# Optimization experiments

Hardware: AMD Instinct MI355X
Metric: run time of the kernel (lower is better)

Reference implementation:

```python
import jax, jax.numpy as jnp
import numpy as np

B, S, DM = 4, 2048, 1024
H, HD = 16, 64  # num_heads, head_dimension


def setup_inputs() -> dict:
    key = jax.random.key(0)
    ks = jax.random.split(key, 11)
    s = 0.02
    return {
        "queries": jax.random.normal(ks[0], (B, S, DM), dtype=jnp.float32),
        "keys": jax.random.normal(ks[1], (B, S, DM), dtype=jnp.float32),
        "values": jax.random.normal(ks[2], (B, S, DM), dtype=jnp.float32),
        # projection params, stored [in, out] (transpose of torch Linear weight)
        "Wq": jax.random.normal(ks[3], (DM, H * HD), dtype=jnp.float32) * s,
        "bq": jnp.zeros((H * HD,), dtype=jnp.float32),
        "Wk": jax.random.normal(ks[4], (DM, H * HD), dtype=jnp.float32) * s,
        "bk": jnp.zeros((H * HD,), dtype=jnp.float32),
        "Wv": jax.random.normal(ks[5], (DM, H * HD), dtype=jnp.float32) * s,
        "bv": jnp.zeros((H * HD,), dtype=jnp.float32),
        "Wo": jax.random.normal(ks[6], (H * HD, DM), dtype=jnp.float32) * s,
        "bo": jnp.zeros((DM,), dtype=jnp.float32),
    }


def reference(queries, keys, values, Wq, bq, Wk, bk, Wv, bv, Wo, bo):
    b, s, _ = queries.shape
    # project and split heads: [b, s, H*HD] -> [b, H, s, HD]
    def split(x):
        return x.reshape(b, s, H, HD).transpose(0, 2, 1, 3)
    q = split(queries @ Wq + bq)
    k = split(keys @ Wk + bk)
    v = split(values @ Wv + bv)
    # raw scores [b, H, sq, sk]
    attn = jnp.einsum("bhqd,bhkd->bhqk", q, k)
    # FAITHFUL to source: mask is a no-op (masked_fill result discarded);
    # softmax over axis=2 (the QUERY axis), then scaled by 1/sqrt(HD) after.
    attn = jax.nn.softmax(attn, axis=2) / jnp.sqrt(jnp.float32(HD))
    out = jnp.einsum("bhqk,bhkd->bhqd", attn, v)  # [b, H, s, HD]
    out = out.transpose(0, 2, 1, 3).reshape(b, s, H * HD)
    return out @ Wo + bo
```

## Files before the change

kernel.cpp:

```cpp
#include <hip/hip_runtime.h>
#include <cstddef>


typedef unsigned short u16t;
typedef __attribute__((ext_vector_type(8))) short short8;
typedef __attribute__((ext_vector_type(4))) float floatx4;

#define MFMA16(a, b, c) __builtin_amdgcn_mfma_f32_16x16x32_bf16((a), (b), (c), 0, 0, 0)
#define GLDS16(g, l)                                                        \
  __builtin_amdgcn_global_load_lds(                                         \
      (const __attribute__((address_space(1))) unsigned int*)(g),           \
      (__attribute__((address_space(3))) unsigned int*)(l), 16, 0, 0)

#if __has_builtin(__builtin_amdgcn_exp2f)
#define EXP2(x) __builtin_amdgcn_exp2f(x)
#else
#define EXP2(x) __expf(0.69314718f * (x))
#endif

static __device__ __forceinline__ u16t f2bf(float f) {
  union { float f; unsigned u; } v; v.f = f;
  unsigned r = v.u + 0x7FFFu + ((v.u >> 16) & 1u);
  return (u16t)(r >> 16);
}
static __device__ __forceinline__ unsigned pack2(float hi, float lo) {
  union { float f; unsigned u; } a, b; a.f = hi; b.f = lo;
  return __builtin_amdgcn_perm(a.u + 0x8000u, b.u + 0x8000u, 0x07060302u);
}

static __device__ __forceinline__ int swz(int row, int col) {
  return (((col >> 3) ^ (row & 7)) << 3) | (col & 7);
}

#define SEQ    2048
#define NHEAD  16
#define HDIM   64
#define DMODEL 1024

__global__ __launch_bounds__(256)
void wt_kernel(const float* __restrict__ W0, const float* __restrict__ W1,
               const float* __restrict__ W2, const float* __restrict__ W3,
               u16t* __restrict__ T0, u16t* __restrict__ T1,
               u16t* __restrict__ T2, u16t* __restrict__ T3) {
  int id = blockIdx.x * 256 + threadIdx.x;
  int wsel = id >> 17;
  int r = id & 131071;
  int n = r & 1023;
  int k0 = (r >> 10) << 3;
  const float* W = wsel == 0 ? W0 : wsel == 1 ? W1 : wsel == 2 ? W2 : W3;
  u16t* T = wsel == 0 ? T0 : wsel == 1 ? T1 : wsel == 2 ? T2 : T3;
  const float* src = W + (size_t)k0 * 1024 + n;
  float f[8];
#pragma unroll
  for (int i = 0; i < 8; ++i) f[i] = src[(size_t)i * 1024];
  uint4 p;
  p.x = pack2(f[1], f[0]); p.y = pack2(f[3], f[2]);
  p.z = pack2(f[5], f[4]); p.w = pack2(f[7], f[6]);
  *(uint4*)&T[(size_t)n * 1024 + (k0 & ~63) + swz(n, k0 & 63)] = p;
}

template <int MODE>
__global__ __launch_bounds__(256)
void gemm_bt(const void* __restrict__ Ap0, const void* __restrict__ Ap1,
             const u16t* __restrict__ BT0, const u16t* __restrict__ BT1,
             const float* __restrict__ bias0, const float* __restrict__ bias1,
             void* __restrict__ Cp0, void* __restrict__ Cp1,
             float sc0, float sc1, const float* __restrict__ sscv) {
  constexpr int K = 1024;
  __shared__ __align__(16) u16t lA[128 * 64];
  __shared__ __align__(16) u16t lB[128 * 64];
  const int z = blockIdx.z;
  const void* Ap = z ? Ap1 : Ap0;
  const u16t* BT = z ? BT1 : BT0;
  const float* bias = z ? bias1 : bias0;
  void* Cp = z ? Cp1 : Cp0;
  const float qsc = z ? sc1 : sc0;
  const int tid = threadIdx.x;
  const int lane = tid & 63, w = tid >> 6;
  const int wm = w >> 1, wn = w & 1;
  const int lrow = lane & 15, lq = lane >> 4;
  const int m0 = blockIdx.y * 128, n0 = blockIdx.x * 128;

  floatx4 acc[4][4];
#pragma unroll
  for (int i = 0; i < 4; ++i)
#pragma unroll
    for (int j = 0; j < 4; ++j) acc[i][j] = {0.f, 0.f, 0.f, 0.f};

  for (int kb = 0; kb < K; kb += 64) {
    if constexpr (MODE == 1) {
      const u16t* Ag = (const u16t*)Ap;
#pragma unroll
      for (int i = 0; i < 4; ++i) {
        int chunk = w * 4 + i;
        int off = chunk * 1024 + lane * 16;
        int r = off >> 7, ib = off & 127;
        GLDS16(Ag + (size_t)(m0 + r) * K + kb + (ib >> 1), &lA[chunk * 512]);
      }
    } else {
      const float* Ag = (const float*)Ap;
#pragma unroll
      for (int i = 0; i < 8; ++i) {
        int e = (i * 256 + tid) * 4;
        int r = e >> 6, c = e & 63;
        const float* src = Ag + (size_t)(m0 + r) * K + kb + c;
        uint2 p;
        p.x = pack2(src[1], src[0]);
        p.y = pack2(src[3], src[2]);
        *(uint2*)&lA[r * 64 + swz(r, c)] = p;
      }
    }
#pragma unroll
    for (int i = 0; i < 4; ++i) {
      int chunk = w * 4 + i;
      int off = chunk * 1024 + lane * 16;
      int r = off >> 7, ib = off & 127;
      GLDS16(BT + (size_t)(n0 + r) * K + kb + (ib >> 1), &lB[chunk * 512]);
    }
    __syncthreads();
#pragma unroll
    for (int kk = 0; kk < 2; ++kk) {
      short8 af[4], bfr[4];
#pragma unroll
      for (int t = 0; t < 4; ++t) {
        int ar = wm * 64 + t * 16 + lrow;
        af[t] = *(const short8*)&lA[ar * 64 + swz(ar, kk * 32 + lq * 8)];
      }
#pragma unroll
      for (int t = 0; t < 4; ++t) {
        int br = wn * 64 + t * 16 + lrow;
        bfr[t] = *(const short8*)&lB[br * 64 + swz(br, kk * 32 + lq * 8)];
      }
#pragma unroll
      for (int i = 0; i < 4; ++i)
#pragma unroll
        for (int j = 0; j < 4; ++j)
          acc[i][j] = MFMA16(af[i], bfr[j], acc[i][j]);
    }
    __syncthreads();
  }

  float bvv[4];
#pragma unroll
  for (int j = 0; j < 4; ++j) bvv[j] = bias[n0 + wn * 64 + j * 16 + lrow];
  const int h = (n0 + wn * 64) >> 6;
#pragma unroll
  for (int i = 0; i < 4; ++i) {
#pragma unroll
    for (int r = 0; r < 4; ++r) {
      int rg = m0 + wm * 64 + i * 16 + lq * 4 + r;
      int b = rg >> 11, s = rg & 2047;
      float rs;
      if constexpr (MODE == 2) rs = sscv[(size_t)(b * NHEAD + h) * SEQ + s];
      else                     rs = qsc;
#pragma unroll
      for (int j = 0; j < 4; ++j) {
        int cg = n0 + wn * 64 + j * 16 + lrow;
        float v = acc[i][j][r] + bvv[j];
        if constexpr (MODE == 1) {
          ((float*)Cp)[(size_t)rg * 1024 + cg] = v;
        } else {
          v *= rs;
          int d = cg & 63;
          size_t bh = (size_t)(b * NHEAD + h);
          if constexpr (MODE == 0)
            ((u16t*)Cp)[(bh * SEQ + s) * HDIM + swz(s, d)] = f2bf(v);
          else
            ((u16t*)Cp)[(bh * HDIM + d) * SEQ + (s & ~127) + swz(d, s & 127)] = f2bf(v);
        }
      }
    }
  }
}

__global__ __launch_bounds__(256)
void stats_kernel(const u16t* __restrict__ Qb, const u16t* __restrict__ Kb,
                  float* __restrict__ ss) {
  __shared__ __align__(16) u16t lK[128 * 64];
  __shared__ __align__(16) u16t lQ[128 * 64];
  const int tid = threadIdx.x, lane = tid & 63, w = tid >> 6;
  const int lrow = lane & 15, lq = lane >> 4;
  const int bh = blockIdx.y;
  const int c0 = blockIdx.x * 128;
  const u16t* Kbase = Kb + (size_t)bh * (SEQ * HDIM);
  const u16t* Qbase = Qb + (size_t)bh * (SEQ * HDIM);

#pragma unroll
  for (int i = 0; i < 4; ++i) {
    int chunk = w * 4 + i;
    GLDS16(Kbase + (size_t)c0 * HDIM + chunk * 512 + lane * 8, &lK[chunk * 512]);
  }

  short8 bfK[4];
  float lcur[2] = {0.f, 0.f};

  for (int q0 = 0; q0 < SEQ; q0 += 128) {
#pragma unroll
    for (int i = 0; i < 4; ++i) {
      int chunk = w * 4 + i;
      GLDS16(Qbase + (size_t)q0 * HDIM + chunk * 512 + lane * 8, &lQ[chunk * 512]);
    }
    __syncthreads();
    if (q0 == 0) {
#pragma unroll
      for (int nt = 0; nt < 2; ++nt) {
        int kr = w * 32 + nt * 16 + lrow;
        bfK[nt * 2]     = *(const short8*)&lK[kr * 64 + swz(kr, lq * 8)];
        bfK[nt * 2 + 1] = *(const short8*)&lK[kr * 64 + swz(kr, lq * 8 + 32)];
      }
    }
#pragma unroll
    for (int mt = 0; mt < 8; ++mt) {
      int qr = mt * 16 + lrow;
      short8 af0 = *(const short8*)&lQ[qr * 64 + swz(qr, lq * 8)];
      short8 af1 = *(const short8*)&lQ[qr * 64 + swz(qr, lq * 8 + 32)];
#pragma unroll
      for (int nt = 0; nt < 2; ++nt) {
        floatx4 a = {0.f, 0.f, 0.f, 0.f};
        a = MFMA16(af0, bfK[nt * 2], a);
        a = MFMA16(af1, bfK[nt * 2 + 1], a);
        lcur[nt] += EXP2(a[0]) + EXP2(a[1]) + EXP2(a[2]) + EXP2(a[3]);
      }
    }
    __syncthreads();
  }
#pragma unroll
  for (int t = 0; t < 2; ++t) {
    float ll = lcur[t];
    ll += __shfl_xor(ll, 16);
    ll += __shfl_xor(ll, 32);
    lcur[t] = ll;
  }
  if (lane < 16) {
#pragma unroll
    for (int t = 0; t < 2; ++t) {
      int col = c0 + w * 32 + t * 16 + lane;
      ss[(size_t)bh * SEQ + col] = 1.f / (8.f * lcur[t]);
    }
  }
}

__global__ __launch_bounds__(256)
void attn_kernel(const u16t* __restrict__ Qb, const u16t* __restrict__ Kb,
                 const u16t* __restrict__ Vt, u16t* __restrict__ Hout) {
  __shared__ __align__(16) u16t lKP[128 * 64];
  __shared__ __align__(16) u16t lV[64 * 128];
  const int tid = threadIdx.x, lane = tid & 63, w = tid >> 6;
  const int lrow = lane & 15, lq = lane >> 4;
  const int bh = blockIdx.y, q0 = blockIdx.x * 64;
  const size_t hb = (size_t)bh * (SEQ * HDIM);

#pragma unroll
  for (int i = 0; i < 2; ++i) {
    int chunk = w * 2 + i;
    GLDS16(Qb + hb + (size_t)q0 * HDIM + chunk * 512 + lane * 8, &lKP[chunk * 512]);
  }
  __syncthreads();
  const int qr = w * 16 + lrow;
  short8 bq0 = *(const short8*)&lKP[qr * 64 + swz(qr, lq * 8)];
  short8 bq1 = *(const short8*)&lKP[qr * 64 + swz(qr, lq * 8 + 32)];
  __syncthreads();

  floatx4 ao[4];
#pragma unroll
  for (int t = 0; t < 4; ++t) ao[t] = {0.f, 0.f, 0.f, 0.f};

  for (int kt = 0; kt < 16; ++kt) {
    const int k0 = kt * 128;
#pragma unroll
    for (int i = 0; i < 4; ++i) {
      int chunk = w * 4 + i;
      GLDS16(Kb + hb + (size_t)k0 * HDIM + chunk * 512 + lane * 8, &lKP[chunk * 512]);
    }
#pragma unroll
    for (int i = 0; i < 4; ++i) {
      int chunk = w * 4 + i;
      int off = chunk * 1024 + lane * 16;
      int d = off >> 8, ib = off & 255;
      GLDS16(Vt + hb + ((size_t)d << 11) + k0 + (ib >> 1), &lV[chunk * 512]);
    }
    __syncthreads();

    floatx4 st[8];
#pragma unroll
    for (int nt = 0; nt < 8; ++nt) {
      int kr = nt * 16 + lrow;
      short8 ak0 = *(const short8*)&lKP[kr * 64 + swz(kr, lq * 8)];
      short8 ak1 = *(const short8*)&lKP[kr * 64 + swz(kr, lq * 8 + 32)];
      floatx4 a = {0.f, 0.f, 0.f, 0.f};
      a = MFMA16(ak0, bq0, a);
      a = MFMA16(ak1, bq1, a);
      st[nt] = a;
    }
    __syncthreads();

#pragma unroll
    for (int nt = 0; nt < 8; ++nt) {
      float p0 = EXP2(st[nt][0]);
      float p1 = EXP2(st[nt][1]);
      float p2 = EXP2(st[nt][2]);
      float p3 = EXP2(st[nt][3]);
      uint2 pk; pk.x = pack2(p1, p0); pk.y = pack2(p3, p2);
      *(uint2*)&lKP[qr * 128 + swz(qr, nt * 16 + lq * 4)] = pk;
    }
    {
      short8 ap[4];
#pragma unroll
      for (int kk = 0; kk < 4; ++kk)
        ap[kk] = *(const short8*)&lKP[qr * 128 + swz(qr, kk * 32 + lq * 8)];
#pragma unroll
      for (int nt = 0; nt < 4; ++nt) {
        int vr = nt * 16 + lrow;
#pragma unroll
        for (int kk = 0; kk < 4; ++kk) {
          short8 bv = *(const short8*)&lV[vr * 128 + swz(vr, kk * 32 + lq * 8)];
          ao[nt] = MFMA16(ap[kk], bv, ao[nt]);
        }
      }
    }
    __syncthreads();
  }

  const int b = bh >> 4, h = bh & 15;
#pragma unroll
  for (int nt = 0; nt < 4; ++nt) {
    int d = nt * 16 + lrow;
#pragma unroll
    for (int r = 0; r < 4; ++r) {
      int q = q0 + w * 16 + lq * 4 + r;
      Hout[((size_t)b * SEQ + q) * DMODEL + h * HDIM + swz(q, d)] = f2bf(ao[nt][r]);
    }
  }
}

extern "C" void kernel_launch(void* const* d_in, const int* in_sizes, int n_in,
                              void* d_out, int out_size, void* d_ws, size_t ws_size,
                              hipStream_t stream) {
  (void)in_sizes; (void)n_in; (void)out_size; (void)ws_size;
  const float* queries = (const float*)d_in[0];
  const float* keys    = (const float*)d_in[1];
  const float* values  = (const float*)d_in[2];
  const float* Wq = (const float*)d_in[3];
  const float* bq = (const float*)d_in[4];
  const float* Wk = (const float*)d_in[5];
  const float* bk = (const float*)d_in[6];
  const float* Wv = (const float*)d_in[7];
  const float* bv = (const float*)d_in[8];
  const float* Wo = (const float*)d_in[9];
  const float* bo = (const float*)d_in[10];

  char* ws = (char*)d_ws;
  const size_t MB = 1024 * 1024;
  u16t* Qb   = (u16t*)(ws + 0 * MB);
  u16t* Kb   = (u16t*)(ws + 16 * MB);
  u16t* Vt   = (u16t*)(ws + 32 * MB);
  u16t* Hout = (u16t*)(ws + 48 * MB);
  u16t* wqt  = (u16t*)(ws + 64 * MB);
  u16t* wkt  = (u16t*)(ws + 66 * MB);
  u16t* wvt  = (u16t*)(ws + 68 * MB);
  u16t* wot  = (u16t*)(ws + 70 * MB);
  float* ssc = (float*)(ws + 72 * MB);

  wt_kernel<<<2048, 256, 0, stream>>>(Wq, Wk, Wv, Wo, wqt, wkt, wvt, wot);

  gemm_bt<0><<<dim3(8, 64, 2), 256, 0, stream>>>(
      queries, keys, wqt, wkt, bq, bk, Qb, Kb, 1.44269504f, 1.0f, nullptr);

  stats_kernel<<<dim3(16, 64), 256, 0, stream>>>(Qb, Kb, ssc);

  gemm_bt<2><<<dim3(8, 64, 1), 256, 0, stream>>>(
      values, values, wvt, wvt, bv, bv, Vt, Vt, 1.0f, 1.0f, ssc);

  attn_kernel<<<dim3(32, 64), 256, 0, stream>>>(Qb, Kb, Vt, Hout);

  gemm_bt<1><<<dim3(8, 64, 1), 256, 0, stream>>>(
      Hout, Hout, wot, wot, bo, bo, d_out, d_out, 1.0f, 1.0f, nullptr);
}
```

Baseline: 443.1 us.

## Fuse QKV projections, use 32x32 MFMA in stats and attention kernels

Merges the Q/K and V projection launches into one three-slice launch and moves the per-key softmax normalizer from the V projection epilogue into the attention kernel, where P is scaled by it before the PV product. Stats and attention kernels switch from 16x16x32 to 32x32x16 bf16 MFMA with larger per-wave tiles, building P fragments in registers via lane shuffles instead of an LDS round trip. Attention splits the key dimension across waves and reduces partial outputs through LDS, with a vectorized output store. This adds more register pressure and an extra reduction step.

```diff
diff --git a/kernel.cpp b/kernel.cpp
--- a/kernel.cpp
+++ b/kernel.cpp
@@ -5,8 +5,10 @@
 typedef unsigned short u16t;
 typedef __attribute__((ext_vector_type(8))) short short8;
 typedef __attribute__((ext_vector_type(4))) float floatx4;
+typedef __attribute__((ext_vector_type(16))) float floatx16;
 
 #define MFMA16(a, b, c) __builtin_amdgcn_mfma_f32_16x16x32_bf16((a), (b), (c), 0, 0, 0)
+#define MFMA32(a, b, c) __builtin_amdgcn_mfma_f32_32x32x16_bf16((a), (b), (c), 0, 0, 0)
 #define GLDS16(g, l)                                                        \
   __builtin_amdgcn_global_load_lds(                                         \
       (const __attribute__((address_space(1))) unsigned int*)(g),           \
@@ -30,6 +32,9 @@
 
 static __device__ __forceinline__ int swz(int row, int col) {
   return (((col >> 3) ^ (row & 7)) << 3) | (col & 7);
+}
+static __device__ __forceinline__ int sw4(int row, int col) {
+  return ((((col >> 2) ^ row) & 15) << 2) | (col & 3);
 }
 
 #define SEQ    2048
@@ -59,22 +64,24 @@
   *(uint4*)&T[(size_t)n * 1024 + (k0 & ~63) + swz(n, k0 & 63)] = p;
 }
 
-template <int MODE>
 __global__ __launch_bounds__(256)
-void gemm_bt(const void* __restrict__ Ap0, const void* __restrict__ Ap1,
-             const u16t* __restrict__ BT0, const u16t* __restrict__ BT1,
-             const float* __restrict__ bias0, const float* __restrict__ bias1,
-             void* __restrict__ Cp0, void* __restrict__ Cp1,
-             float sc0, float sc1, const float* __restrict__ sscv) {
+void proj_qkv(const float* __restrict__ Aq, const float* __restrict__ Ak,
+              const float* __restrict__ Av,
+              const u16t* __restrict__ Wq, const u16t* __restrict__ Wk,
+              const u16t* __restrict__ Wv,
+              const float* __restrict__ Bq, const float* __restrict__ Bk,
+              const float* __restrict__ Bv,
+              u16t* __restrict__ Oq, u16t* __restrict__ Ok,
+              u16t* __restrict__ Ov) {
   constexpr int K = 1024;
   __shared__ __align__(16) u16t lA[128 * 64];
   __shared__ __align__(16) u16t lB[128 * 64];
   const int z = blockIdx.z;
-  const void* Ap = z ? Ap1 : Ap0;
-  const u16t* BT = z ? BT1 : BT0;
-  const float* bias = z ? bias1 : bias0;
-  void* Cp = z ? Cp1 : Cp0;
-  const float qsc = z ? sc1 : sc0;
+  const float* Ap = z == 0 ? Aq : z == 1 ? Ak : Av;
+  const u16t* BT = z == 0 ? Wq : z == 1 ? Wk : Wv;
+  const float* bias = z == 0 ? Bq : z == 1 ? Bk : Bv;
+  u16t* Cp = z == 0 ? Oq : z == 1 ? Ok : Ov;
+  const float qsc = z == 0 ? 1.44269504f : 1.0f;
   const int tid = threadIdx.x;
   const int lane = tid & 63, w = tid >> 6;
   const int wm = w >> 1, wn = w & 1;
@@ -88,27 +95,15 @@
     for (int j = 0; j < 4; ++j) acc[i][j] = {0.f, 0.f, 0.f, 0.f};
 
   for (int kb = 0; kb < K; kb += 64) {
-    if constexpr (MODE == 1) {
-      const u16t* Ag = (const u16t*)Ap;
-#pragma unroll
-      for (int i = 0; i < 4; ++i) {
-        int chunk = w * 4 + i;
-        int off = chunk * 1024 + lane * 16;
-        int r = off >> 7, ib = off & 127;
-        GLDS16(Ag + (size_t)(m0 + r) * K + kb + (ib >> 1), &lA[chunk * 512]);
-      }
-    } else {
-      const float* Ag = (const float*)Ap;
-#pragma unroll
-      for (int i = 0; i < 8; ++i) {
-        int e = (i * 256 + tid) * 4;
-        int r = e >> 6, c = e & 63;
-        const float* src = Ag + (size_t)(m0 + r) * K + kb + c;
-        uint2 p;
-        p.x = pack2(src[1], src[0]);
-        p.y = pack2(src[3], src[2]);
-        *(uint2*)&lA[r * 64 + swz(r, c)] = p;
-      }
+#pragma unroll
+    for (int i = 0; i < 8; ++i) {
+      int e = (i * 256 + tid) * 4;
+      int r = e >> 6, c = e & 63;
+      const float* src = Ap + (size_t)(m0 + r) * K + kb + c;
+      uint2 p;
+      p.x = pack2(src[1], src[0]);
+      p.y = pack2(src[3], src[2]);
+      *(uint2*)&lA[r * 64 + swz(r, c)] = p;
     }
 #pragma unroll
     for (int i = 0; i < 4; ++i) {
@@ -150,187 +145,343 @@
     for (int r = 0; r < 4; ++r) {
       int rg = m0 + wm * 64 + i * 16 + lq * 4 + r;
       int b = rg >> 11, s = rg & 2047;
-      float rs;
-      if constexpr (MODE == 2) rs = sscv[(size_t)(b * NHEAD + h) * SEQ + s];
-      else                     rs = qsc;
+      size_t bh = (size_t)(b * NHEAD + h);
 #pragma unroll
       for (int j = 0; j < 4; ++j) {
         int cg = n0 + wn * 64 + j * 16 + lrow;
-        float v = acc[i][j][r] + bvv[j];
-        if constexpr (MODE == 1) {
-          ((float*)Cp)[(size_t)rg * 1024 + cg] = v;
-        } else {
-          v *= rs;
-          int d = cg & 63;
-          size_t bh = (size_t)(b * NHEAD + h);
-          if constexpr (MODE == 0)
-            ((u16t*)Cp)[(bh * SEQ + s) * HDIM + swz(s, d)] = f2bf(v);
-          else
-            ((u16t*)Cp)[(bh * HDIM + d) * SEQ + (s & ~127) + swz(d, s & 127)] = f2bf(v);
-        }
-      }
-    }
-  }
+        int d = cg & 63;
+        float v = (acc[i][j][r] + bvv[j]) * qsc;
+        if (z < 2)
+          Cp[(bh * SEQ + s) * HDIM + swz(s, d)] = f2bf(v);
+        else
+          Cp[(bh * HDIM + d) * SEQ + (s & ~127) + swz(d, s & 127)] = f2bf(v);
+      }
+    }
+  }
+}
+
+__global__ __launch_bounds__(256)
+void proj_out(const u16t* __restrict__ Ap, const u16t* __restrict__ BT,
+              const float* __restrict__ bias, float* __restrict__ Cp) {
+  constexpr int K = 1024;
+  __shared__ __align__(16) u16t lA[128 * 64];
+  __shared__ __align__(16) u16t lB[128 * 64];
+  const int tid = threadIdx.x;
+  const int lane = tid & 63, w = tid >> 6;
+  const int wm = w >> 1, wn = w & 1;
+  const int lrow = lane & 15, lq = lane >> 4;
+  const int m0 = blockIdx.y * 128, n0 = blockIdx.x * 128;
+
+  floatx4 acc[4][4];
+#pragma unroll
+  for (int i = 0; i < 4; ++i)
+#pragma unroll
+    for (int j = 0; j < 4; ++j) acc[i][j] = {0.f, 0.f, 0.f, 0.f};
+
+  for (int kb = 0; kb < K; kb += 64) {
+#pragma unroll
+    for (int i = 0; i < 4; ++i) {
+      int chunk = w * 4 + i;
+      int off = chunk * 1024 + lane * 16;
+      int r = off >> 7, ib = off & 127;
+      GLDS16(Ap + (size_t)(m0 + r) * K + kb + (ib >> 1), &lA[chunk * 512]);
+    }
+#pragma unroll
+    for (int i = 0; i < 4; ++i) {
+      int chunk = w * 4 + i;
+      int off = chunk * 1024 + lane * 16;
+      int r = off >> 7, ib = off & 127;
+      GLDS16(BT + (size_t)(n0 + r) * K + kb + (ib >> 1), &lB[chunk * 512]);
+    }
+    __syncthreads();
+#pragma unroll
+    for (int kk = 0; kk < 2; ++kk) {
+      short8 af[4], bfr[4];
+#pragma unroll
+      for (int t = 0; t < 4; ++t) {
+        int ar = wm * 64 + t * 16 + lrow;
+        af[t] = *(const short8*)&lA[ar * 64 + swz(ar, kk * 32 + lq * 8)];
+      }
+#pragma unroll
+      for (int t = 0; t < 4; ++t) {
+        int br = wn * 64 + t * 16 + lrow;
+        bfr[t] = *(const short8*)&lB[br * 64 + swz(br, kk * 32 + lq * 8)];
+      }
+#pragma unroll
+      for (int i = 0; i < 4; ++i)
+#pragma unroll
+        for (int j = 0; j < 4; ++j)
+          acc[i][j] = MFMA16(af[i], bfr[j], acc[i][j]);
+    }
+    __syncthreads();
+  }
+
+  float bvv[4];
+#pragma unroll
+  for (int j = 0; j < 4; ++j) bvv[j] = bias[n0 + wn * 64 + j * 16 + lrow];
+#pragma unroll
+  for (int i = 0; i < 4; ++i)
+#pragma unroll
+    for (int r = 0; r < 4; ++r) {
+      int rg = m0 + wm * 64 + i * 16 + lq * 4 + r;
+#pragma unroll
+      for (int j = 0; j < 4; ++j) {
+        int cg = n0 + wn * 64 + j * 16 + lrow;
+        Cp[(size_t)rg * 1024 + cg] = acc[i][j][r] + bvv[j];
+      }
+    }
 }
 
 __global__ __launch_bounds__(256)
 void stats_kernel(const u16t* __restrict__ Qb, const u16t* __restrict__ Kb,
                   float* __restrict__ ss) {
-  __shared__ __align__(16) u16t lK[128 * 64];
+  __shared__ __align__(16) u16t lK[256 * 64];
   __shared__ __align__(16) u16t lQ[128 * 64];
   const int tid = threadIdx.x, lane = tid & 63, w = tid >> 6;
-  const int lrow = lane & 15, lq = lane >> 4;
+  const int l31 = lane & 31, lh = lane >> 5;
   const int bh = blockIdx.y;
-  const int c0 = blockIdx.x * 128;
+  const int c0 = blockIdx.x * 256;
   const u16t* Kbase = Kb + (size_t)bh * (SEQ * HDIM);
   const u16t* Qbase = Qb + (size_t)bh * (SEQ * HDIM);
 
 #pragma unroll
-  for (int i = 0; i < 4; ++i) {
-    int chunk = w * 4 + i;
-    GLDS16(Kbase + (size_t)c0 * HDIM + chunk * 512 + lane * 8, &lK[chunk * 512]);
-  }
-
-  short8 bfK[4];
-  float lcur[2] = {0.f, 0.f};
+  for (int i = 0; i < 8; ++i) {
+    int c = w * 8 + i;
+    GLDS16(Kbase + (size_t)c0 * HDIM + c * 512 + lane * 8, &lK[c * 512]);
+  }
+
+  short8 kf[2][4];
+  float acc[2][16];
+#pragma unroll
+  for (int kb = 0; kb < 2; ++kb)
+#pragma unroll
+    for (int r = 0; r < 16; ++r) acc[kb][r] = 0.f;
 
   for (int q0 = 0; q0 < SEQ; q0 += 128) {
 #pragma unroll
     for (int i = 0; i < 4; ++i) {
-      int chunk = w * 4 + i;
-      GLDS16(Qbase + (size_t)q0 * HDIM + chunk * 512 + lane * 8, &lQ[chunk * 512]);
+      int c = w * 4 + i;
+      GLDS16(Qbase + (size_t)q0 * HDIM + c * 512 + lane * 8, &lQ[c * 512]);
     }
     __syncthreads();
     if (q0 == 0) {
 #pragma unroll
-      for (int nt = 0; nt < 2; ++nt) {
-        int kr = w * 32 + nt * 16 + lrow;
-        bfK[nt * 2]     = *(const short8*)&lK[kr * 64 + swz(kr, lq * 8)];
-        bfK[nt * 2 + 1] = *(const short8*)&lK[kr * 64 + swz(kr, lq * 8 + 32)];
-      }
-    }
-#pragma unroll
-    for (int mt = 0; mt < 8; ++mt) {
-      int qr = mt * 16 + lrow;
-      short8 af0 = *(const short8*)&lQ[qr * 64 + swz(qr, lq * 8)];
-      short8 af1 = *(const short8*)&lQ[qr * 64 + swz(qr, lq * 8 + 32)];
-#pragma unroll
-      for (int nt = 0; nt < 2; ++nt) {
-        floatx4 a = {0.f, 0.f, 0.f, 0.f};
-        a = MFMA16(af0, bfK[nt * 2], a);
-        a = MFMA16(af1, bfK[nt * 2 + 1], a);
-        lcur[nt] += EXP2(a[0]) + EXP2(a[1]) + EXP2(a[2]) + EXP2(a[3]);
-      }
-    }
-    __syncthreads();
-  }
-#pragma unroll
-  for (int t = 0; t < 2; ++t) {
-    float ll = lcur[t];
-    ll += __shfl_xor(ll, 16);
-    ll += __shfl_xor(ll, 32);
-    lcur[t] = ll;
-  }
-  if (lane < 16) {
-#pragma unroll
-    for (int t = 0; t < 2; ++t) {
-      int col = c0 + w * 32 + t * 16 + lane;
-      ss[(size_t)bh * SEQ + col] = 1.f / (8.f * lcur[t]);
-    }
+      for (int kb = 0; kb < 2; ++kb)
+#pragma unroll
+        for (int t = 0; t < 4; ++t) {
+          int r = w * 64 + kb * 32 + l31;
+          kf[kb][t] = *(const short8*)&lK[r * 64 + swz(r, t * 16 + lh * 8)];
+        }
+    }
+#pragma unroll
+    for (int qb = 0; qb < 4; ++qb) {
+      short8 qfr[4];
+#pragma unroll
+      for (int t = 0; t < 4; ++t) {
+        int r = qb * 32 + l31;
+        qfr[t] = *(const short8*)&lQ[r * 64 + swz(r, t * 16 + lh * 8)];
+      }
+#pragma unroll
+      for (int kb = 0; kb < 2; ++kb) {
+        floatx16 st;
+#pragma unroll
+        for (int r = 0; r < 16; ++r) st[r] = 0.f;
+#pragma unroll
+        for (int t = 0; t < 4; ++t) st = MFMA32(kf[kb][t], qfr[t], st);
+#pragma unroll
+        for (int r = 0; r < 16; ++r) acc[kb][r] += EXP2(st[r]);
+      }
+    }
+    __syncthreads();
+  }
+#pragma unroll
+  for (int kb = 0; kb < 2; ++kb)
+#pragma unroll
+    for (int r = 0; r < 16; ++r) {
+      float v = acc[kb][r];
+#pragma unroll
+      for (int off = 1; off <= 16; off <<= 1) v += __shfl_xor(v, off);
+      acc[kb][r] = v;
+    }
+  if (l31 == 0) {
+#pragma unroll
+    for (int kb = 0; kb < 2; ++kb)
+#pragma unroll
+      for (int r = 0; r < 16; ++r) {
+        int k = c0 + w * 64 + kb * 32 + (r & 3) + 8 * (r >> 2) + 4 * lh;
+        ss[(size_t)bh * SEQ + k] = 1.f / (8.f * acc[kb][r]);
+      }
   }
 }
 
 __global__ __launch_bounds__(256)
 void attn_kernel(const u16t* __restrict__ Qb, const u16t* __restrict__ Kb,
-                 const u16t* __restrict__ Vt, u16t* __restrict__ Hout) {
-  __shared__ __align__(16) u16t lKP[128 * 64];
-  __shared__ __align__(16) u16t lV[64 * 128];
+                 const u16t* __restrict__ Vt, const float* __restrict__ ssc,
+                 u16t* __restrict__ Hout) {
+  __shared__ __align__(16) u16t lbuf[128 * 64 + 64 * 128];
+  u16t* lK = lbuf;
+  u16t* lV = lbuf + 128 * 64;
   const int tid = threadIdx.x, lane = tid & 63, w = tid >> 6;
-  const int lrow = lane & 15, lq = lane >> 4;
+  const int l31 = lane & 31, lh = lane >> 5;
   const int bh = blockIdx.y, q0 = blockIdx.x * 64;
   const size_t hb = (size_t)bh * (SEQ * HDIM);
+  const float* ssb = ssc + (size_t)bh * SEQ;
 
 #pragma unroll
   for (int i = 0; i < 2; ++i) {
-    int chunk = w * 2 + i;
-    GLDS16(Qb + hb + (size_t)q0 * HDIM + chunk * 512 + lane * 8, &lKP[chunk * 512]);
+    int c = w * 2 + i;
+    GLDS16(Qb + hb + (size_t)q0 * HDIM + c * 512 + lane * 8, &lK[c * 512]);
   }
   __syncthreads();
-  const int qr = w * 16 + lrow;
-  short8 bq0 = *(const short8*)&lKP[qr * 64 + swz(qr, lq * 8)];
-  short8 bq1 = *(const short8*)&lKP[qr * 64 + swz(qr, lq * 8 + 32)];
+  short8 qf[2][4];
+#pragma unroll
+  for (int qb = 0; qb < 2; ++qb)
+#pragma unroll
+    for (int t = 0; t < 4; ++t) {
+      int r = qb * 32 + l31;
+      qf[qb][t] = *(const short8*)&lK[r * 64 + swz(r, t * 16 + lh * 8)];
+    }
   __syncthreads();
 
-  floatx4 ao[4];
-#pragma unroll
-  for (int t = 0; t < 4; ++t) ao[t] = {0.f, 0.f, 0.f, 0.f};
+  floatx16 oacc[2][2];
+#pragma unroll
+  for (int a = 0; a < 2; ++a)
+#pragma unroll
+    for (int b = 0; b < 2; ++b)
+#pragma unroll
+      for (int r = 0; r < 16; ++r) oacc[a][b][r] = 0.f;
 
   for (int kt = 0; kt < 16; ++kt) {
     const int k0 = kt * 128;
 #pragma unroll
     for (int i = 0; i < 4; ++i) {
-      int chunk = w * 4 + i;
-      GLDS16(Kb + hb + (size_t)k0 * HDIM + chunk * 512 + lane * 8, &lKP[chunk * 512]);
+      int c = w * 4 + i;
+      GLDS16(Kb + hb + (size_t)k0 * HDIM + c * 512 + lane * 8, &lK[c * 512]);
     }
 #pragma unroll
     for (int i = 0; i < 4; ++i) {
-      int chunk = w * 4 + i;
-      int off = chunk * 1024 + lane * 16;
+      int c = w * 4 + i;
+      int off = c * 1024 + lane * 16;
       int d = off >> 8, ib = off & 255;
-      GLDS16(Vt + hb + ((size_t)d << 11) + k0 + (ib >> 1), &lV[chunk * 512]);
-    }
-    __syncthreads();
-
-    floatx4 st[8];
-#pragma unroll
-    for (int nt = 0; nt < 8; ++nt) {
-      int kr = nt * 16 + lrow;
-      short8 ak0 = *(const short8*)&lKP[kr * 64 + swz(kr, lq * 8)];
-      short8 ak1 = *(const short8*)&lKP[kr * 64 + swz(kr, lq * 8 + 32)];
-      floatx4 a = {0.f, 0.f, 0.f, 0.f};
-      a = MFMA16(ak0, bq0, a);
-      a = MFMA16(ak1, bq1, a);
-      st[nt] = a;
-    }
-    __syncthreads();
-
-#pragma unroll
-    for (int nt = 0; nt < 8; ++nt) {
-      float p0 = EXP2(st[nt][0]);
-      float p1 = EXP2(st[nt][1]);
-      float p2 = EXP2(st[nt][2]);
-      float p3 = EXP2(st[nt][3]);
-      uint2 pk; pk.x = pack2(p1, p0); pk.y = pack2(p3, p2);
-      *(uint2*)&lKP[qr * 128 + swz(qr, nt * 16 + lq * 4)] = pk;
-    }
-    {
-      short8 ap[4];
-#pragma unroll
-      for (int kk = 0; kk < 4; ++kk)
-        ap[kk] = *(const short8*)&lKP[qr * 128 + swz(qr, kk * 32 + lq * 8)];
-#pragma unroll
-      for (int nt = 0; nt < 4; ++nt) {
-        int vr = nt * 16 + lrow;
-#pragma unroll
-        for (int kk = 0; kk < 4; ++kk) {
-          short8 bv = *(const short8*)&lV[vr * 128 + swz(vr, kk * 32 + lq * 8)];
-          ao[nt] = MFMA16(ap[kk], bv, ao[nt]);
+      GLDS16(Vt + hb + ((size_t)d << 11) + k0 + (ib >> 1), &lV[c * 512]);
+    }
+    float4 sv[4];
+#pragma unroll
+    for (int g = 0; g < 4; ++g)
+      sv[g] = *(const float4*)&ssb[k0 + w * 32 + g * 8 + lh * 4];
+    __syncthreads();
+
+    short8 kf[4];
+#pragma unroll
+    for (int t = 0; t < 4; ++t) {
+      int r = w * 32 + l31;
+      kf[t] = *(const short8*)&lK[r * 64 + swz(r, t * 16 + lh * 8)];
+    }
+
+    short8 pfrag[2][2];
+#pragma unroll
+    for (int qb = 0; qb < 2; ++qb) {
+      floatx16 st;
+#pragma unroll
+      for (int r = 0; r < 16; ++r) st[r] = 0.f;
+#pragma unroll
+      for (int t = 0; t < 4; ++t) st = MFMA32(kf[t], qf[qb][t], st);
+      unsigned G[8];
+#pragma unroll
+      for (int g = 0; g < 4; ++g) {
+        float p0 = EXP2(st[g * 4 + 0]) * sv[g].x;
+        float p1 = EXP2(st[g * 4 + 1]) * sv[g].y;
+        float p2 = EXP2(st[g * 4 + 2]) * sv[g].z;
+        float p3 = EXP2(st[g * 4 + 3]) * sv[g].w;
+        G[g * 2] = pack2(p1, p0);
+        G[g * 2 + 1] = pack2(p3, p2);
+      }
+#pragma unroll
+      for (int tt = 0; tt < 2; ++tt) {
+        unsigned aA = G[tt * 4 + 0], bA = G[tt * 4 + 1];
+        unsigned aB = G[tt * 4 + 2], bB = G[tt * 4 + 3];
+        unsigned paA = (unsigned)__shfl_xor((int)aA, 32);
+        unsigned pbA = (unsigned)__shfl_xor((int)bA, 32);
+        unsigned paB = (unsigned)__shfl_xor((int)aB, 32);
+        unsigned pbB = (unsigned)__shfl_xor((int)bB, 32);
+        union { unsigned u[4]; short8 s; } t4;
+        t4.u[0] = lh ? paB : aA;
+        t4.u[1] = lh ? pbB : bA;
+        t4.u[2] = lh ? aB : paA;
+        t4.u[3] = lh ? bB : pbA;
+        pfrag[qb][tt] = t4.s;
+      }
+    }
+#pragma unroll
+    for (int db = 0; db < 2; ++db) {
+      short8 vf[2];
+#pragma unroll
+      for (int tt = 0; tt < 2; ++tt) {
+        int r = db * 32 + l31;
+        vf[tt] = *(const short8*)&lV[r * 128 + swz(r, w * 32 + tt * 16 + lh * 8)];
+      }
+#pragma unroll
+      for (int qb = 0; qb < 2; ++qb)
+#pragma unroll
+        for (int tt = 0; tt < 2; ++tt)
+          oacc[db][qb] = MFMA32(vf[tt], pfrag[qb][tt], oacc[db][qb]);
+    }
+    __syncthreads();
+  }
+
+  float* R0 = (float*)lbuf;
+  float* R1 = (float*)(lbuf + 128 * 64);
+  if (w < 2) {
+    float* R = w ? R1 : R0;
+#pragma unroll
+    for (int db = 0; db < 2; ++db)
+#pragma unroll
+      for (int qb = 0; qb < 2; ++qb)
+#pragma unroll
+        for (int g = 0; g < 4; ++g) {
+          int q = qb * 32 + l31, d = db * 32 + g * 8 + lh * 4;
+          float4 v;
+          v.x = oacc[db][qb][g * 4 + 0]; v.y = oacc[db][qb][g * 4 + 1];
+          v.z = oacc[db][qb][g * 4 + 2]; v.w = oacc[db][qb][g * 4 + 3];
+          *(float4*)&R[q * 64 + sw4(q, d)] = v;
         }
-      }
-    }
-    __syncthreads();
-  }
-
+  }
+  __syncthreads();
+  if (w >= 2) {
+    float* R = (w == 3) ? R1 : R0;
+#pragma unroll
+    for (int db = 0; db < 2; ++db)
+#pragma unroll
+      for (int qb = 0; qb < 2; ++qb)
+#pragma unroll
+        for (int g = 0; g < 4; ++g) {
+          int q = qb * 32 + l31, d = db * 32 + g * 8 + lh * 4;
+          float4* p = (float4*)&R[q * 64 + sw4(q, d)];
+          float4 v = *p;
+          v.x += oacc[db][qb][g * 4 + 0]; v.y += oacc[db][qb][g * 4 + 1];
+          v.z += oacc[db][qb][g * 4 + 2]; v.w += oacc[db][qb][g * 4 + 3];
+          *p = v;
+        }
+  }
+  __syncthreads();
   const int b = bh >> 4, h = bh & 15;
-#pragma unroll
-  for (int nt = 0; nt < 4; ++nt) {
-    int d = nt * 16 + lrow;
-#pragma unroll
-    for (int r = 0; r < 4; ++r) {
-      int q = q0 + w * 16 + lq * 4 + r;
-      Hout[((size_t)b * SEQ + q) * DMODEL + h * HDIM + swz(q, d)] = f2bf(ao[nt][r]);
-    }
-  }
+  const int q = tid >> 2, dc = (tid & 3) * 16;
+  float4 o[4];
+#pragma unroll
+  for (int i = 0; i < 4; ++i) {
+    float4 x = *(const float4*)&R0[q * 64 + sw4(q, dc + i * 4)];
+    float4 y = *(const float4*)&R1[q * 64 + sw4(q, dc + i * 4)];
+    o[i].x = x.x + y.x; o[i].y = x.y + y.y;
+    o[i].z = x.z + y.z; o[i].w = x.w + y.w;
+  }
+  size_t row = ((size_t)b * SEQ + q0 + q) * DMODEL + h * HDIM;
+  uint4 u0, u1;
+  u0.x = pack2(o[0].y, o[0].x); u0.y = pack2(o[0].w, o[0].z);
+  u0.z = pack2(o[1].y, o[1].x); u0.w = pack2(o[1].w, o[1].z);
+  u1.x = pack2(o[2].y, o[2].x); u1.y = pack2(o[2].w, o[2].z);
+  u1.z = pack2(o[3].y, o[3].x); u1.w = pack2(o[3].w, o[3].z);
+  *(uint4*)&Hout[row + swz(q, dc)] = u0;
+  *(uint4*)&Hout[row + swz(q, dc + 8)] = u1;
 }
 
 extern "C" void kernel_launch(void* const* d_in, const int* in_sizes, int n_in,
@@ -363,16 +514,12 @@
 
   wt_kernel<<<2048, 256, 0, stream>>>(Wq, Wk, Wv, Wo, wqt, wkt, wvt, wot);
 
-  gemm_bt<0><<<dim3(8, 64, 2), 256, 0, stream>>>(
-      queries, keys, wqt, wkt, bq, bk, Qb, Kb, 1.44269504f, 1.0f, nullptr);
-
-  stats_kernel<<<dim3(16, 64), 256, 0, stream>>>(Qb, Kb, ssc);
-
-  gemm_bt<2><<<dim3(8, 64, 1), 256, 0, stream>>>(
-      values, values, wvt, wvt, bv, bv, Vt, Vt, 1.0f, 1.0f, ssc);
-
-  attn_kernel<<<dim3(32, 64), 256, 0, stream>>>(Qb, Kb, Vt, Hout);
-
-  gemm_bt<1><<<dim3(8, 64, 1), 256, 0, stream>>>(
-      Hout, Hout, wot, wot, bo, bo, d_out, d_out, 1.0f, 1.0f, nullptr);
-}
+  proj_qkv<<<dim3(8, 64, 3), 256, 0, stream>>>(
+      queries, keys, values, wqt, wkt, wvt, bq, bk, bv, Qb, Kb, Vt);
+
+  stats_kernel<<<dim3(8, 64), 256, 0, stream>>>(Qb, Kb, ssc);
+
+  attn_kernel<<<dim3(32, 64), 256, 0, stream>>>(Qb, Kb, Vt, ssc, Hout);
+
+  proj_out<<<dim3(8, 64), 256, 0, stream>>>(Hout, wot, bo, (float*)d_out);
+}
```

After: 497.4 us. +12.3%, slower.
